# Kernel optimization log

Hardware: AMD Instinct MI355X
Metric: run time of the kernel (lower is better)

The kernel has to match this reference:

```python
import jax, jax.numpy as jnp
import numpy as np

B, T, V, E, U = 1024, 128, 32000, 128, 512


def setup_inputs() -> dict:
    key = jax.random.key(0)
    ks = jax.random.split(key, 8)
    s = lambda k, *sh: jax.random.normal(k, sh, dtype=jnp.float32) * 0.05
    return {
        "tokens": jax.random.randint(ks[0], (B, T), 0, V, dtype=jnp.int32),
        "emb": s(ks[1], V, E),
        "Wx0": s(ks[2], E, U),
        "Wh0": s(ks[3], U, U),
        "b0": jnp.zeros((U,), jnp.float32),
        "Wx1": s(ks[4], U, U),
        "Wh1": s(ks[5], U, U),
        "b1": jnp.zeros((U,), jnp.float32),
        "Wo": s(ks[6], U, 1),
        "bo": jnp.zeros((1,), jnp.float32),
    }


def reference(tokens, emb, Wx0, Wh0, b0, Wx1, Wh1, b1, Wo, bo):
    # Embedding lookup: [B, T, E]
    x = emb[tokens]
    xs = jnp.swapaxes(x, 0, 1)  # [T, B, E] for time-major scan
    h0 = jnp.zeros((tokens.shape[0], Wh0.shape[0]), x.dtype)
    h1 = jnp.zeros((tokens.shape[0], Wh1.shape[0]), x.dtype)

    def step(carry, xt):
        h0, h1 = carry
        # SimpleRNNCell layer 0: h' = tanh(x@Wx + h@Wh + b)
        h0 = jnp.tanh(xt @ Wx0 + h0 @ Wh0 + b0)
        # SimpleRNNCell layer 1 stacked on out0
        h1 = jnp.tanh(h0 @ Wx1 + h1 @ Wh1 + b1)
        return (h0, h1), None

    (h0, h1), _ = jax.lax.scan(step, (h0, h1), xs)
    logits = h1 @ Wo + bo            # [B, 1]
    return jax.nn.sigmoid(logits)
```

## Files before the change

### kernel.cpp

```cpp
#include <hip/hip_runtime.h>
#include <hip/hip_bf16.h>

#define B_ 1024
#define T_ 128
#define E_ 128
#define U_ 512
#define V_ 32000
#define NC 16
#define NG 16
#define MB 64
#define NB 32
#define HS ((size_t)B_ * U_)

#define CTR_OFF 0
#define XMASK_OFF (512u << 10)
#define FH0_OFF (520u << 10)
#define FH1_OFF (528u << 10)
#define H0H_OFF (1u << 20)
#define H0L_OFF (3u << 20)
#define H1H_OFF (5u << 20)
#define H1L_OFF (7u << 20)
#define EMBW_OFF (9u << 20)
#define ZERO_BYTES (9u << 20)

typedef unsigned int uint32;
typedef __bf16 bf16x8 __attribute__((ext_vector_type(8)));
typedef float f32x4 __attribute__((ext_vector_type(4)));
typedef unsigned short us8 __attribute__((ext_vector_type(8)));

#define MFMA __builtin_amdgcn_mfma_f32_16x16x32_bf16

__device__ __forceinline__ unsigned short f2b(float f) {
  uint32 u = __builtin_bit_cast(uint32, f);
  u += 0x7fffu + ((u >> 16) & 1u);
  return (unsigned short)(u >> 16);
}
__device__ __forceinline__ float b2f(unsigned short h) {
  return __builtin_bit_cast(float, (uint32)h << 16);
}

__device__ __forceinline__ bf16x8 lds_frag(const unsigned short* s, int row, int k, int K) {
  uint32 off = (uint32)((row * K + k) * 2) ^ (uint32)((row & 7) << 4);
  us8 v = *(const us8*)((const char*)s + off);
  return __builtin_bit_cast(bf16x8, v);
}
__device__ __forceinline__ bf16x8 g_frag(const unsigned short* p) {
  us8 v = *(const us8*)p;
  return __builtin_bit_cast(bf16x8, v);
}
__device__ __forceinline__ void st_coh(unsigned short* p, unsigned short v) {
  __hip_atomic_store(p, v, __ATOMIC_RELAXED, __HIP_MEMORY_SCOPE_AGENT);
}
template <bool FAST>
__device__ __forceinline__ void st_h(unsigned short* p, unsigned short v) {
  if (FAST) *p = v; else st_coh(p, v);
}

template <bool FAST>
__device__ __forceinline__ void wave_signal(uint32* f, uint32 val, int lane) {
  asm volatile("s_waitcnt vmcnt(0)" ::: "memory");
  if (lane == 0) {
    if (FAST) *(volatile uint32*)f = val;
    else __hip_atomic_store(f, val, __ATOMIC_RELAXED, __HIP_MEMORY_SCOPE_AGENT);
  }
}

template <bool FAST>
__device__ __forceinline__ void wave_wait(const uint32* f0, const uint32* f1,
                                          int t, int lane) {
  if (t == 0) return;
  const uint32 tgt = (lane < 16) ? (uint32)t : ((lane < 32) ? (uint32)(t - 1) : 0u);
  const uint32* p = (lane < 16) ? (f0 + lane) : (f1 + (lane & 15));
  while (true) {
    uint32 v;
    if (FAST) v = *(const volatile uint32*)p;
    else v = __hip_atomic_load(p, __ATOMIC_RELAXED, __HIP_MEMORY_SCOPE_AGENT);
    if (__all(v >= tgt)) break;
    if (FAST) asm volatile("buffer_inv" ::: "memory");
    __builtin_amdgcn_s_sleep(2);
  }
  if (FAST) asm volatile("buffer_inv\n\ts_waitcnt vmcnt(0)" ::: "memory");
  else __builtin_amdgcn_fence(__ATOMIC_ACQUIRE, "agent");
}

__device__ __forceinline__ void bar_agent(uint32* ctr, int phase, int g, int tid) {
  asm volatile("s_waitcnt vmcnt(0)" ::: "memory");
  __syncthreads();
  if (tid == 0) {
    uint32* a = &ctr[(uint32)((phase << 4) | g) << 4];
    __hip_atomic_fetch_add(a, 1u, __ATOMIC_RELAXED, __HIP_MEMORY_SCOPE_AGENT);
    while (__hip_atomic_load(a, __ATOMIC_RELAXED, __HIP_MEMORY_SCOPE_AGENT) < NC)
      __builtin_amdgcn_s_sleep(1);
    __builtin_amdgcn_fence(__ATOMIC_ACQUIRE, "agent");
  }
  __syncthreads();
}

__global__ void rnn_init(unsigned char* ws) {
  const uint4 z = {0u, 0u, 0u, 0u};
  uint4* p = (uint4*)ws;
  size_t n = ZERO_BYTES / 16;
  for (size_t j = (size_t)blockIdx.x * blockDim.x + threadIdx.x; j < n;
       j += (size_t)gridDim.x * blockDim.x)
    p[j] = z;
}

__global__ __launch_bounds__(256) void embw_gemm(const float* __restrict__ emb,
                                                 const float* __restrict__ Wx0,
                                                 unsigned short* __restrict__ embW) {
  const int tid = threadIdx.x;
  const int lane = tid & 63;
  const int wv = tid >> 6;
  const int arow = lane & 15;
  const int kgrp = (lane >> 4) * 8;
  const int vrow = blockIdx.x * 64 + wv * 16;

  bf16x8 a[4];
  for (int kt = 0; kt < 4; ++kt) {
    const float* p = emb + (size_t)(vrow + arow) * E_ + kt * 32 + kgrp;
    float4 f0 = ((const float4*)p)[0];
    float4 f1 = ((const float4*)p)[1];
    us8 u;
    u[0] = f2b(f0.x); u[1] = f2b(f0.y); u[2] = f2b(f0.z); u[3] = f2b(f0.w);
    u[4] = f2b(f1.x); u[5] = f2b(f1.y); u[6] = f2b(f1.z); u[7] = f2b(f1.w);
    a[kt] = __builtin_bit_cast(bf16x8, u);
  }
  const int c0 = blockIdx.y * 64;
  for (int nt = 0; nt < 4; ++nt) {
    const int col = c0 + nt * 16 + (lane & 15);
    f32x4 acc = {0.f, 0.f, 0.f, 0.f};
    for (int kt = 0; kt < 4; ++kt) {
      us8 ub;
      for (int j = 0; j < 8; ++j)
        ub[j] = f2b(Wx0[(size_t)(kt * 32 + kgrp + j) * U_ + col]);
      acc = MFMA(a[kt], __builtin_bit_cast(bf16x8, ub), acc, 0, 0, 0);
    }
    const int crow = vrow + (lane >> 4) * 4;
    for (int i = 0; i < 4; ++i)
      embW[(size_t)(crow + i) * U_ + col] = f2b(acc[i]);
  }
}

template <bool FAST>
__device__ __forceinline__ void rnn_loop(
    const int* __restrict__ tokens, const unsigned short* __restrict__ embW,
    unsigned short* h0h, unsigned short* h0l, unsigned short* h1h,
    unsigned short* h1l, const uint32* f0w, const uint32* f1w, uint32* myF0,
    uint32* myF1, const unsigned short* sWh0h, const unsigned short* sWh0l,
    const unsigned short* sWx1h, const unsigned short* sWh1h,
    const unsigned short* sWh1l, int r0, int c0, int lane, int rowB, int kgrp,
    int rowA, float b0v0, float b0v1, float b1v0, float b1v1) {
  const int l15 = lane & 15;
  const float b0a[2] = {b0v0, b0v1};
  const float b1a[2] = {b1v0, b1v1};

  unsigned short embP[2][4];
#pragma unroll
  for (int nt = 0; nt < 2; ++nt)
    for (int i = 0; i < 4; ++i) {
      int tk = tokens[(size_t)(r0 + rowB + i) * T_ + 0];
      embP[nt][i] = embW[(size_t)tk * U_ + c0 + nt * 16 + l15];
    }

  for (int t = 0; t <= T_; ++t) {
    wave_wait<FAST>(f0w, f1w, t, lane);

    const size_t rb0 = (size_t)((t & 1) ^ 1) * HS;
    bf16x8 h0h_r[16], h0l_r[16];
    {
      const unsigned short* aph = h0h + rb0 + (size_t)rowA * U_ + kgrp;
      const unsigned short* apl = h0l + rb0 + (size_t)rowA * U_ + kgrp;
#pragma unroll
      for (int kt = 0; kt < 16; ++kt) {
        h0h_r[kt] = g_frag(aph + kt * 32);
        h0l_r[kt] = g_frag(apl + kt * 32);
      }
    }
    bf16x8 a1h_r[16], a1l_r[16];
    if (t >= 1) {
      const size_t rb1 = (size_t)(t & 1) * HS;
      const unsigned short* a1h = h1h + rb1 + (size_t)rowA * U_ + kgrp;
      const unsigned short* a1l = h1l + rb1 + (size_t)rowA * U_ + kgrp;
#pragma unroll
      for (int kt = 0; kt < 16; ++kt) {
        a1h_r[kt] = g_frag(a1h + kt * 32);
        a1l_r[kt] = g_frag(a1l + kt * 32);
      }
    }
    unsigned short embN[2][4];
    if (t + 1 < T_) {
#pragma unroll
      for (int nt = 0; nt < 2; ++nt)
        for (int i = 0; i < 4; ++i) {
          int tk = tokens[(size_t)(r0 + rowB + i) * T_ + (t + 1)];
          embN[nt][i] = embW[(size_t)tk * U_ + c0 + nt * 16 + l15];
        }
    }

    if (t < T_) {
      const size_t wbuf = (size_t)(t & 1) * HS;
#pragma unroll
      for (int nt = 0; nt < 2; ++nt) {
        const int colL = nt * 16 + l15;
        f32x4 aC, aD = {0.f, 0.f, 0.f, 0.f};
        for (int i = 0; i < 4; ++i) aC[i] = b0a[nt] + b2f(embP[nt][i]);
#pragma unroll
        for (int kt = 0; kt < 16; ++kt) {
          bf16x8 bh = lds_frag(sWh0h, colL, kt * 32 + kgrp, U_);
          bf16x8 bl = lds_frag(sWh0l, colL, kt * 32 + kgrp, U_);
          aC = MFMA(h0h_r[kt], bh, aC, 0, 0, 0);
          aD = MFMA(h0l_r[kt], bh, aD, 0, 0, 0);
          aD = MFMA(h0h_r[kt], bl, aD, 0, 0, 0);
        }
        size_t ob = wbuf + (size_t)(r0 + rowB) * U_ + (c0 + colL);
        for (int i = 0; i < 4; ++i) {
          float v = tanhf(aC[i] + aD[i]);
          unsigned short hi = f2b(v);
          st_h<FAST>(&h0h[ob + (size_t)i * U_], hi);
          st_h<FAST>(&h0l[ob + (size_t)i * U_], f2b(v - b2f(hi)));
        }
      }
      wave_signal<FAST>(myF0, (uint32)(t + 1), lane);
    }

    if (t >= 1) {
      const size_t wb1 = (size_t)((t - 1) & 1) * HS;
#pragma unroll
      for (int nt = 0; nt < 2; ++nt) {
        const int colL = nt * 16 + l15;
        f32x4 aA = {0.f, 0.f, 0.f, 0.f};
        f32x4 aB = {b1a[nt], b1a[nt], b1a[nt], b1a[nt]};
#pragma unroll
        for (int kt = 0; kt < 16; ++kt) {
          bf16x8 bxh = lds_frag(sWx1h, colL, kt * 32 + kgrp, U_);
          aA = MFMA(h0h_r[kt], bxh, aA, 0, 0, 0);
          aA = MFMA(h0l_r[kt], bxh, aA, 0, 0, 0);
          bf16x8 bh = lds_frag(sWh1h, colL, kt * 32 + kgrp, U_);
          aB = MFMA(a1h_r[kt], bh, aB, 0, 0, 0);
          aB = MFMA(a1l_r[kt], bh, aB, 0, 0, 0);
          if (kt < 15) {
            bf16x8 bl = lds_frag(sWh1l, colL, kt * 32 + kgrp, 480);
            aB = MFMA(a1h_r[kt], bl, aB, 0, 0, 0);
          }
        }
        size_t ob = wb1 + (size_t)(r0 + rowB) * U_ + (c0 + colL);
        for (int i = 0; i < 4; ++i) {
          float v = tanhf(aA[i] + aB[i]);
          unsigned short hi = f2b(v);
          st_h<FAST>(&h1h[ob + (size_t)i * U_], hi);
          st_h<FAST>(&h1l[ob + (size_t)i * U_], f2b(v - b2f(hi)));
        }
      }
      wave_signal<FAST>(myF1, (uint32)t, lane);
    }

    if (t + 1 < T_) {
#pragma unroll
      for (int nt = 0; nt < 2; ++nt)
        for (int i = 0; i < 4; ++i) embP[nt][i] = embN[nt][i];
    }
  }
}

__global__ __launch_bounds__(256, 1) void rnn_main(
    const int* __restrict__ tokens, const float* __restrict__ b0,
    const float* __restrict__ Wh0, const float* __restrict__ Wx1,
    const float* __restrict__ Wh1, const float* __restrict__ b1,
    unsigned char* ws) {
  __shared__ unsigned short sWh0h[NB * U_];
  __shared__ unsigned short sWh0l[NB * U_];
  __shared__ unsigned short sWx1h[NB * U_];
  __shared__ unsigned short sWh1h[NB * U_];
  __shared__ unsigned short sWh1l[NB * 480];
  __shared__ uint32 sFast;

  const int tid = threadIdx.x;
  const int bid = blockIdx.x;
  const int g = bid & (NG - 1);
  const int c = bid >> 4;
  const int r0 = g * MB;
  const int c0 = c * NB;

  uint32* ctr = (uint32*)(ws + CTR_OFF);
  uint32* fH0 = (uint32*)(ws + FH0_OFF);
  uint32* fH1 = (uint32*)(ws + FH1_OFF);
  unsigned short* h0h = (unsigned short*)(ws + H0H_OFF);
  unsigned short* h0l = (unsigned short*)(ws + H0L_OFF);
  unsigned short* h1h = (unsigned short*)(ws + H1H_OFF);
  unsigned short* h1l = (unsigned short*)(ws + H1L_OFF);
  const unsigned short* embW = (const unsigned short*)(ws + EMBW_OFF);

  for (int idx = tid; idx < NB * U_; idx += 256) {
    int cl = idx & 31, k = idx >> 5;
    float v = Wh0[(size_t)k * U_ + c0 + cl];
    unsigned short hi = f2b(v);
    uint32 off = (uint32)((cl * U_ + k) * 2) ^ (uint32)((cl & 7) << 4);
    *(unsigned short*)((char*)sWh0h + off) = hi;
    *(unsigned short*)((char*)sWh0l + off) = f2b(v - b2f(hi));
  }
  for (int idx = tid; idx < NB * U_; idx += 256) {
    int cl = idx & 31, k = idx >> 5;
    float v = Wx1[(size_t)k * U_ + c0 + cl];
    uint32 off = (uint32)((cl * U_ + k) * 2) ^ (uint32)((cl & 7) << 4);
    *(unsigned short*)((char*)sWx1h + off) = f2b(v);
  }
  for (int idx = tid; idx < NB * U_; idx += 256) {
    int cl = idx & 31, k = idx >> 5;
    float v = Wh1[(size_t)k * U_ + c0 + cl];
    unsigned short hi = f2b(v);
    uint32 off = (uint32)((cl * U_ + k) * 2) ^ (uint32)((cl & 7) << 4);
    *(unsigned short*)((char*)sWh1h + off) = hi;
    if (k < 480) {
      uint32 offl = (uint32)((cl * 480 + k) * 2) ^ (uint32)((cl & 7) << 4);
      *(unsigned short*)((char*)sWh1l + offl) = f2b(v - b2f(hi));
    }
  }

  {
    uint32 xcd;
    asm volatile("s_getreg_b32 %0, hwreg(HW_REG_XCC_ID)" : "=s"(xcd));
    uint32* xm = (uint32*)(ws + XMASK_OFF) + (uint32)g * 16;
    if (tid == 0)
      __hip_atomic_fetch_or(xm, 1u << (xcd & 31u), __ATOMIC_RELAXED,
                            __HIP_MEMORY_SCOPE_AGENT);
    bar_agent(ctr, T_, g, tid);
    if (tid == 0) {
      uint32 m = __hip_atomic_load(xm, __ATOMIC_RELAXED, __HIP_MEMORY_SCOPE_AGENT);
      sFast = (__popc(m) == 1) ? 1u : 0u;
    }
  }

  const int lane = tid & 63;
  const int mt = tid >> 6;
  const int l15 = lane & 15;
  const int rowB = mt * 16 + ((lane >> 4) << 2);
  const int kgrp = (lane >> 4) * 8;
  const int rowA = r0 + mt * 16 + l15;
  const float b0v0 = b0[c0 + l15], b0v1 = b0[c0 + 16 + l15];
  const float b1v0 = b1[c0 + l15], b1v1 = b1[c0 + 16 + l15];

  const uint32* f0w = fH0 + (((uint32)g * 4 + mt) << 4);
  const uint32* f1w = fH1 + (((uint32)g * 4 + mt) << 4);
  uint32* myF0 = (uint32*)f0w + c;
  uint32* myF1 = (uint32*)f1w + c;

  __syncthreads();
  const bool fast = (sFast != 0);

  if (fast)
    rnn_loop<true>(tokens, embW, h0h, h0l, h1h, h1l, f0w, f1w, myF0, myF1,
                   sWh0h, sWh0l, sWx1h, sWh1h, sWh1l, r0, c0, lane, rowB, kgrp,
                   rowA, b0v0, b0v1, b1v0, b1v1);
  else
    rnn_loop<false>(tokens, embW, h0h, h0l, h1h, h1l, f0w, f1w, myF0, myF1,
                    sWh0h, sWh0l, sWx1h, sWh1h, sWh1l, r0, c0, lane, rowB, kgrp,
                    rowA, b0v0, b0v1, b1v0, b1v1);
}

__global__ void rnn_final(const unsigned short* __restrict__ h1h,
                          const unsigned short* __restrict__ h1l,
                          const float* __restrict__ Wo,
                          const float* __restrict__ bo, float* __restrict__ out) {
  int lane = threadIdx.x & 63;
  int b = blockIdx.x * 4 + (threadIdx.x >> 6);
  us8 hh = *(const us8*)(h1h + (size_t)b * U_ + lane * 8);
  us8 hl = *(const us8*)(h1l + (size_t)b * U_ + lane * 8);
  const float4* wp = (const float4*)(Wo + lane * 8);
  float4 w0 = wp[0], w1 = wp[1];
  float s = (b2f(hh[0]) + b2f(hl[0])) * w0.x + (b2f(hh[1]) + b2f(hl[1])) * w0.y +
            (b2f(hh[2]) + b2f(hl[2])) * w0.z + (b2f(hh[3]) + b2f(hl[3])) * w0.w +
            (b2f(hh[4]) + b2f(hl[4])) * w1.x + (b2f(hh[5]) + b2f(hl[5])) * w1.y +
            (b2f(hh[6]) + b2f(hl[6])) * w1.z + (b2f(hh[7]) + b2f(hl[7])) * w1.w;
  for (int off = 32; off > 0; off >>= 1) s += __shfl_down(s, off, 64);
  if (lane == 0) out[b] = 1.0f / (1.0f + expf(-(s + bo[0])));
}

extern "C" void kernel_launch(void* const* d_in, const int* in_sizes, int n_in,
                              void* d_out, int out_size, void* d_ws, size_t ws_size,
                              hipStream_t stream) {
  const int* tokens = (const int*)d_in[0];
  const float* emb = (const float*)d_in[1];
  const float* Wx0 = (const float*)d_in[2];
  const float* Wh0 = (const float*)d_in[3];
  const float* b0 = (const float*)d_in[4];
  const float* Wx1 = (const float*)d_in[5];
  const float* Wh1 = (const float*)d_in[6];
  const float* b1 = (const float*)d_in[7];
  const float* Wo = (const float*)d_in[8];
  const float* bo = (const float*)d_in[9];
  unsigned char* ws = (unsigned char*)d_ws;
  float* out = (float*)d_out;

  hipLaunchKernelGGL(rnn_init, dim3(1024), dim3(256), 0, stream, ws);
  hipLaunchKernelGGL(embw_gemm, dim3(V_ / 64, U_ / 64), dim3(256), 0, stream,
                     emb, Wx0, (unsigned short*)(ws + EMBW_OFF));
  hipLaunchKernelGGL(rnn_main, dim3(NC * NG), dim3(256), 0, stream, tokens,
                     b0, Wh0, Wx1, Wh1, b1, ws);
  hipLaunchKernelGGL(rnn_final, dim3(256), dim3(256), 0, stream,
                     (const unsigned short*)(ws + H1H_OFF) + (size_t)1 * B_ * U_,
                     (const unsigned short*)(ws + H1L_OFF) + (size_t)1 * B_ * U_,
                     Wo, bo, out);
}
```

Before: 2.384 ms.

## Split layer-0 and layer-1 into separate wave roles with triple-buffered h0

```diff
diff --git a/kernel.cpp b/kernel.cpp
--- a/kernel.cpp
+++ b/kernel.cpp
@@ -17,11 +17,11 @@
 #define FH0_OFF (520u << 10)
 #define FH1_OFF (528u << 10)
 #define H0H_OFF (1u << 20)
-#define H0L_OFF (3u << 20)
-#define H1H_OFF (5u << 20)
-#define H1L_OFF (7u << 20)
-#define EMBW_OFF (9u << 20)
-#define ZERO_BYTES (9u << 20)
+#define H0L_OFF (4u << 20)
+#define H1H_OFF (7u << 20)
+#define H1L_OFF (9u << 20)
+#define EMBW_OFF (11u << 20)
+#define ZERO_BYTES (11u << 20)
 
 typedef unsigned int uint32;
 typedef __bf16 bf16x8 __attribute__((ext_vector_type(8)));
@@ -65,12 +65,15 @@
   }
 }
 
-template <bool FAST>
+template <bool FAST, int DLT>
 __device__ __forceinline__ void wave_wait(const uint32* f0, const uint32* f1,
                                           int t, int lane) {
   if (t == 0) return;
-  const uint32 tgt = (lane < 16) ? (uint32)t : ((lane < 32) ? (uint32)(t - 1) : 0u);
-  const uint32* p = (lane < 16) ? (f0 + lane) : (f1 + (lane & 15));
+  const int t1 = t - DLT;
+  const uint32 tgt = (lane < 16) ? (uint32)t
+                                 : ((lane < 32 && t1 > 0) ? (uint32)t1 : 0u);
+  const uint32* p = (lane < 16) ? (f0 + lane)
+                                : ((lane < 32) ? (f1 + (lane & 15)) : f0);
   while (true) {
     uint32 v;
     if (FAST) v = *(const volatile uint32*)p;
@@ -142,18 +145,14 @@
 }
 
 template <bool FAST>
-__device__ __forceinline__ void rnn_loop(
+__device__ __forceinline__ void l0_loop(
     const int* __restrict__ tokens, const unsigned short* __restrict__ embW,
-    unsigned short* h0h, unsigned short* h0l, unsigned short* h1h,
-    unsigned short* h1l, const uint32* f0w, const uint32* f1w, uint32* myF0,
-    uint32* myF1, const unsigned short* sWh0h, const unsigned short* sWh0l,
-    const unsigned short* sWx1h, const unsigned short* sWh1h,
-    const unsigned short* sWh1l, int r0, int c0, int lane, int rowB, int kgrp,
-    int rowA, float b0v0, float b0v1, float b1v0, float b1v1) {
+    unsigned short* h0h, unsigned short* h0l, const uint32* f0w,
+    const uint32* f1w, uint32* myF0, const unsigned short* sWh0h,
+    const unsigned short* sWh0l, int r0, int c0, int lane, int rowB, int kgrp,
+    int rowA, float b0v0, float b0v1) {
   const int l15 = lane & 15;
   const float b0a[2] = {b0v0, b0v1};
-  const float b1a[2] = {b1v0, b1v1};
-
   unsigned short embP[2][4];
 #pragma unroll
   for (int nt = 0; nt < 2; ++nt)
@@ -162,107 +161,131 @@
       embP[nt][i] = embW[(size_t)tk * U_ + c0 + nt * 16 + l15];
     }
 
-  for (int t = 0; t <= T_; ++t) {
-    wave_wait<FAST>(f0w, f1w, t, lane);
-
-    const size_t rb0 = (size_t)((t & 1) ^ 1) * HS;
-    bf16x8 h0h_r[16], h0l_r[16];
+  for (int t = 0; t < T_; ++t) {
+    wave_wait<FAST, 2>(f0w, f1w, t, lane);
+
+    const size_t rb = (size_t)((t + 2) % 3) * HS;
+    bf16x8 hh[16], hl[16];
     {
-      const unsigned short* aph = h0h + rb0 + (size_t)rowA * U_ + kgrp;
-      const unsigned short* apl = h0l + rb0 + (size_t)rowA * U_ + kgrp;
+      const unsigned short* ph = h0h + rb + (size_t)rowA * U_ + kgrp;
+      const unsigned short* pl = h0l + rb + (size_t)rowA * U_ + kgrp;
 #pragma unroll
       for (int kt = 0; kt < 16; ++kt) {
-        h0h_r[kt] = g_frag(aph + kt * 32);
-        h0l_r[kt] = g_frag(apl + kt * 32);
-      }
-    }
-    bf16x8 a1h_r[16], a1l_r[16];
-    if (t >= 1) {
-      const size_t rb1 = (size_t)(t & 1) * HS;
-      const unsigned short* a1h = h1h + rb1 + (size_t)rowA * U_ + kgrp;
-      const unsigned short* a1l = h1l + rb1 + (size_t)rowA * U_ + kgrp;
+        hh[kt] = g_frag(ph + kt * 32);
+        hl[kt] = g_frag(pl + kt * 32);
+      }
+    }
+    const size_t wb = (size_t)(t % 3) * HS;
+#pragma unroll
+    for (int nt = 0; nt < 2; ++nt) {
+      const int colL = nt * 16 + l15;
+      f32x4 aC, aD = {0.f, 0.f, 0.f, 0.f};
+      for (int i = 0; i < 4; ++i) aC[i] = b0a[nt] + b2f(embP[nt][i]);
 #pragma unroll
       for (int kt = 0; kt < 16; ++kt) {
-        a1h_r[kt] = g_frag(a1h + kt * 32);
-        a1l_r[kt] = g_frag(a1l + kt * 32);
-      }
-    }
-    unsigned short embN[2][4];
+        bf16x8 bh = lds_frag(sWh0h, colL, kt * 32 + kgrp, U_);
+        bf16x8 bl = lds_frag(sWh0l, colL, kt * 32 + kgrp, U_);
+        aC = MFMA(hh[kt], bh, aC, 0, 0, 0);
+        aD = MFMA(hl[kt], bh, aD, 0, 0, 0);
+        aD = MFMA(hh[kt], bl, aD, 0, 0, 0);
+      }
+      size_t ob = wb + (size_t)(r0 + rowB) * U_ + (c0 + colL);
+      for (int i = 0; i < 4; ++i) {
+        float v = tanhf(aC[i] + aD[i]);
+        unsigned short hi = f2b(v);
+        st_h<FAST>(&h0h[ob + (size_t)i * U_], hi);
+        st_h<FAST>(&h0l[ob + (size_t)i * U_], f2b(v - b2f(hi)));
+      }
+    }
+    wave_signal<FAST>(myF0, (uint32)(t + 1), lane);
+
     if (t + 1 < T_) {
 #pragma unroll
       for (int nt = 0; nt < 2; ++nt)
         for (int i = 0; i < 4; ++i) {
           int tk = tokens[(size_t)(r0 + rowB + i) * T_ + (t + 1)];
-          embN[nt][i] = embW[(size_t)tk * U_ + c0 + nt * 16 + l15];
+          embP[nt][i] = embW[(size_t)tk * U_ + c0 + nt * 16 + l15];
         }
     }
-
-    if (t < T_) {
-      const size_t wbuf = (size_t)(t & 1) * HS;
+  }
+}
+
+template <bool FAST>
+__device__ __forceinline__ void l1_loop(
+    unsigned short* h0h, unsigned short* h0l, unsigned short* h1h,
+    unsigned short* h1l, const uint32* f0w, const uint32* f1w, uint32* myF1,
+    const unsigned short* sWx1h, const unsigned short* sWh1h,
+    const unsigned short* sWh1l, int r0, int c0, int lane, int rowB, int kgrp,
+    int rowA, float b1v0, float b1v1) {
+  const int l15 = lane & 15;
+  const float b1a[2] = {b1v0, b1v1};
+
+  for (int w = 1; w <= T_; ++w) {
+    wave_wait<FAST, 1>(f0w, f1w, w, lane);
+
+    f32x4 aB[2];
+    {
+      const size_t rb1 = (size_t)(w & 1) * HS;
+      bf16x8 ah[16], al[16];
+      const unsigned short* p1h = h1h + rb1 + (size_t)rowA * U_ + kgrp;
+      const unsigned short* p1l = h1l + rb1 + (size_t)rowA * U_ + kgrp;
+#pragma unroll
+      for (int kt = 0; kt < 16; ++kt) {
+        ah[kt] = g_frag(p1h + kt * 32);
+        al[kt] = g_frag(p1l + kt * 32);
+      }
 #pragma unroll
       for (int nt = 0; nt < 2; ++nt) {
         const int colL = nt * 16 + l15;
-        f32x4 aC, aD = {0.f, 0.f, 0.f, 0.f};
-        for (int i = 0; i < 4; ++i) aC[i] = b0a[nt] + b2f(embP[nt][i]);
+        f32x4 acc = {b1a[nt], b1a[nt], b1a[nt], b1a[nt]};
 #pragma unroll
         for (int kt = 0; kt < 16; ++kt) {
-          bf16x8 bh = lds_frag(sWh0h, colL, kt * 32 + kgrp, U_);
-          bf16x8 bl = lds_frag(sWh0l, colL, kt * 32 + kgrp, U_);
-          aC = MFMA(h0h_r[kt], bh, aC, 0, 0, 0);
-          aD = MFMA(h0l_r[kt], bh, aD, 0, 0, 0);
-          aD = MFMA(h0h_r[kt], bl, aD, 0, 0, 0);
-        }
-        size_t ob = wbuf + (size_t)(r0 + rowB) * U_ + (c0 + colL);
-        for (int i = 0; i < 4; ++i) {
-          float v = tanhf(aC[i] + aD[i]);
-          unsigned short hi = f2b(v);
-          st_h<FAST>(&h0h[ob + (size_t)i * U_], hi);
-          st_h<FAST>(&h0l[ob + (size_t)i * U_], f2b(v - b2f(hi)));
-        }
-      }
-      wave_signal<FAST>(myF0, (uint32)(t + 1), lane);
-    }
-
-    if (t >= 1) {
-      const size_t wb1 = (size_t)((t - 1) & 1) * HS;
-#pragma unroll
-      for (int nt = 0; nt < 2; ++nt) {
-        const int colL = nt * 16 + l15;
-        f32x4 aA = {0.f, 0.f, 0.f, 0.f};
-        f32x4 aB = {b1a[nt], b1a[nt], b1a[nt], b1a[nt]};
-#pragma unroll
-        for (int kt = 0; kt < 16; ++kt) {
-          bf16x8 bxh = lds_frag(sWx1h, colL, kt * 32 + kgrp, U_);
-          aA = MFMA(h0h_r[kt], bxh, aA, 0, 0, 0);
-          aA = MFMA(h0l_r[kt], bxh, aA, 0, 0, 0);
           bf16x8 bh = lds_frag(sWh1h, colL, kt * 32 + kgrp, U_);
-          aB = MFMA(a1h_r[kt], bh, aB, 0, 0, 0);
-          aB = MFMA(a1l_r[kt], bh, aB, 0, 0, 0);
+          acc = MFMA(ah[kt], bh, acc, 0, 0, 0);
+          acc = MFMA(al[kt], bh, acc, 0, 0, 0);
           if (kt < 15) {
             bf16x8 bl = lds_frag(sWh1l, colL, kt * 32 + kgrp, 480);
-            aB = MFMA(a1h_r[kt], bl, aB, 0, 0, 0);
+            acc = MFMA(ah[kt], bl, acc, 0, 0, 0);
           }
         }
-        size_t ob = wb1 + (size_t)(r0 + rowB) * U_ + (c0 + colL);
-        for (int i = 0; i < 4; ++i) {
-          float v = tanhf(aA[i] + aB[i]);
-          unsigned short hi = f2b(v);
-          st_h<FAST>(&h1h[ob + (size_t)i * U_], hi);
-          st_h<FAST>(&h1l[ob + (size_t)i * U_], f2b(v - b2f(hi)));
-        }
-      }
-      wave_signal<FAST>(myF1, (uint32)t, lane);
-    }
-
-    if (t + 1 < T_) {
-#pragma unroll
-      for (int nt = 0; nt < 2; ++nt)
-        for (int i = 0; i < 4; ++i) embP[nt][i] = embN[nt][i];
-    }
-  }
-}
-
-__global__ __launch_bounds__(256, 1) void rnn_main(
+        aB[nt] = acc;
+      }
+    }
+    const size_t rb0 = (size_t)((w + 2) % 3) * HS;
+    bf16x8 hh[16], hl[16];
+    {
+      const unsigned short* ph = h0h + rb0 + (size_t)rowA * U_ + kgrp;
+      const unsigned short* pl = h0l + rb0 + (size_t)rowA * U_ + kgrp;
+#pragma unroll
+      for (int kt = 0; kt < 16; ++kt) {
+        hh[kt] = g_frag(ph + kt * 32);
+        hl[kt] = g_frag(pl + kt * 32);
+      }
+    }
+    const size_t wb1 = (size_t)((w - 1) & 1) * HS;
+#pragma unroll
+    for (int nt = 0; nt < 2; ++nt) {
+      const int colL = nt * 16 + l15;
+      f32x4 aA = {0.f, 0.f, 0.f, 0.f};
+#pragma unroll
+      for (int kt = 0; kt < 16; ++kt) {
+        bf16x8 bxh = lds_frag(sWx1h, colL, kt * 32 + kgrp, U_);
+        aA = MFMA(hh[kt], bxh, aA, 0, 0, 0);
+        aA = MFMA(hl[kt], bxh, aA, 0, 0, 0);
+      }
+      size_t ob = wb1 + (size_t)(r0 + rowB) * U_ + (c0 + colL);
+      for (int i = 0; i < 4; ++i) {
+        float v = tanhf(aA[i] + aB[nt][i]);
+        unsigned short hi = f2b(v);
+        st_h<FAST>(&h1h[ob + (size_t)i * U_], hi);
+        st_h<FAST>(&h1l[ob + (size_t)i * U_], f2b(v - b2f(hi)));
+      }
+    }
+    wave_signal<FAST>(myF1, (uint32)w, lane);
+  }
+}
+
+__global__ __launch_bounds__(512, 2) void rnn_main(
     const int* __restrict__ tokens, const float* __restrict__ b0,
     const float* __restrict__ Wh0, const float* __restrict__ Wx1,
     const float* __restrict__ Wh1, const float* __restrict__ b1,
@@ -290,7 +313,7 @@
   unsigned short* h1l = (unsigned short*)(ws + H1L_OFF);
   const unsigned short* embW = (const unsigned short*)(ws + EMBW_OFF);
 
-  for (int idx = tid; idx < NB * U_; idx += 256) {
+  for (int idx = tid; idx < NB * U_; idx += 512) {
     int cl = idx & 31, k = idx >> 5;
     float v = Wh0[(size_t)k * U_ + c0 + cl];
     unsigned short hi = f2b(v);
@@ -298,13 +321,13 @@
     *(unsigned short*)((char*)sWh0h + off) = hi;
     *(unsigned short*)((char*)sWh0l + off) = f2b(v - b2f(hi));
   }
-  for (int idx = tid; idx < NB * U_; idx += 256) {
+  for (int idx = tid; idx < NB * U_; idx += 512) {
     int cl = idx & 31, k = idx >> 5;
     float v = Wx1[(size_t)k * U_ + c0 + cl];
     uint32 off = (uint32)((cl * U_ + k) * 2) ^ (uint32)((cl & 7) << 4);
     *(unsigned short*)((char*)sWx1h + off) = f2b(v);
   }
-  for (int idx = tid; idx < NB * U_; idx += 256) {
+  for (int idx = tid; idx < NB * U_; idx += 512) {
     int cl = idx & 31, k = idx >> 5;
     float v = Wh1[(size_t)k * U_ + c0 + cl];
     unsigned short hi = f2b(v);
@@ -331,13 +354,13 @@
   }
 
   const int lane = tid & 63;
-  const int mt = tid >> 6;
+  const int wv = tid >> 6;
+  const int mt = wv & 3;
+  const int role = wv >> 2;
   const int l15 = lane & 15;
   const int rowB = mt * 16 + ((lane >> 4) << 2);
   const int kgrp = (lane >> 4) * 8;
   const int rowA = r0 + mt * 16 + l15;
-  const float b0v0 = b0[c0 + l15], b0v1 = b0[c0 + 16 + l15];
-  const float b1v0 = b1[c0 + l15], b1v1 = b1[c0 + 16 + l15];
 
   const uint32* f0w = fH0 + (((uint32)g * 4 + mt) << 4);
   const uint32* f1w = fH1 + (((uint32)g * 4 + mt) << 4);
@@ -347,14 +370,23 @@
   __syncthreads();
   const bool fast = (sFast != 0);
 
-  if (fast)
-    rnn_loop<true>(tokens, embW, h0h, h0l, h1h, h1l, f0w, f1w, myF0, myF1,
-                   sWh0h, sWh0l, sWx1h, sWh1h, sWh1l, r0, c0, lane, rowB, kgrp,
-                   rowA, b0v0, b0v1, b1v0, b1v1);
-  else
-    rnn_loop<false>(tokens, embW, h0h, h0l, h1h, h1l, f0w, f1w, myF0, myF1,
-                    sWh0h, sWh0l, sWx1h, sWh1h, sWh1l, r0, c0, lane, rowB, kgrp,
-                    rowA, b0v0, b0v1, b1v0, b1v1);
+  if (role == 0) {
+    const float b0v0 = b0[c0 + l15], b0v1 = b0[c0 + 16 + l15];
+    if (fast)
+      l0_loop<true>(tokens, embW, h0h, h0l, f0w, f1w, myF0, sWh0h, sWh0l, r0,
+                    c0, lane, rowB, kgrp, rowA, b0v0, b0v1);
+    else
+      l0_loop<false>(tokens, embW, h0h, h0l, f0w, f1w, myF0, sWh0h, sWh0l, r0,
+                     c0, lane, rowB, kgrp, rowA, b0v0, b0v1);
+  } else {
+    const float b1v0 = b1[c0 + l15], b1v1 = b1[c0 + 16 + l15];
+    if (fast)
+      l1_loop<true>(h0h, h0l, h1h, h1l, f0w, f1w, myF1, sWx1h, sWh1h, sWh1l,
+                    r0, c0, lane, rowB, kgrp, rowA, b1v0, b1v1);
+    else
+      l1_loop<false>(h0h, h0l, h1h, h1l, f0w, f1w, myF1, sWx1h, sWh1h, sWh1l,
+                     r0, c0, lane, rowB, kgrp, rowA, b1v0, b1v1);
+  }
 }
 
 __global__ void rnn_final(const unsigned short* __restrict__ h1h,
@@ -394,7 +426,7 @@
   hipLaunchKernelGGL(rnn_init, dim3(1024), dim3(256), 0, stream, ws);
   hipLaunchKernelGGL(embw_gemm, dim3(V_ / 64, U_ / 64), dim3(256), 0, stream,
                      emb, Wx0, (unsigned short*)(ws + EMBW_OFF));
-  hipLaunchKernelGGL(rnn_main, dim3(NC * NG), dim3(256), 0, stream, tokens,
+  hipLaunchKernelGGL(rnn_main, dim3(NC * NG), dim3(512), 0, stream, tokens,
                      b0, Wh0, Wx1, Wh1, b1, ws);
   hipLaunchKernelGGL(rnn_final, dim3(256), dim3(256), 0, stream,
                      (const unsigned short*)(ws + H1H_OFF) + (size_t)1 * B_ * U_,
```

Measured after the change: 2.576 ms. 8.1% more time.
